# Optimization experiments

Hardware: AMD Instinct MI355X
Metric: run time of the kernel (lower is better)

Reference implementation:

```python
import jax, jax.numpy as jnp
import numpy as np

B, NQ, NV, DIM, HEADS, K = 2, 2048, 2048, 256, 8, 8
HD = DIM // HEADS
HID = 4 * DIM
SCALE = HD ** -0.5
EPS = 1e-5


def setup_inputs() -> dict:
    key = jax.random.key(0)
    ks = jax.random.split(key, 40)
    r = lambda i, s: jax.random.normal(ks[i], s, jnp.float32) * 0.02
    inp = {
        'q': jax.random.normal(ks[0], (B, NQ, DIM), jnp.float32),
        'v': jax.random.normal(ks[1], (B, NV, DIM), jnp.float32),
        'q_pos': jax.random.normal(ks[2], (B, NQ, 3), jnp.float32),
        'v_pos': jax.random.normal(ks[3], (B, NV, 3), jnp.float32),
        'self_knn_index': jax.random.randint(ks[4], (B, NQ, K), 0, NQ, jnp.int32),
        'cross_knn_index': jax.random.randint(ks[5], (B, NQ, K), 0, NV, jnp.int32),
        # LayerNorms (gamma=1, beta=0)
        'norm1_g': jnp.ones(DIM), 'norm1_b': jnp.zeros(DIM),
        'normq_g': jnp.ones(DIM), 'normq_b': jnp.zeros(DIM),
        'normv_g': jnp.ones(DIM), 'normv_b': jnp.zeros(DIM),
        'norm2_g': jnp.ones(DIM), 'norm2_b': jnp.zeros(DIM),
        # self-attention (qkv_bias=False), proj has bias
        'sa_qkv_w': r(6, (DIM, 3 * DIM)),
        'sa_proj_w': r(7, (DIM, DIM)), 'sa_proj_b': jnp.zeros(DIM),
        # cross-attention: q proj and kv proj (no bias), out proj with bias
        'ca_q_w': r(8, (DIM, DIM)),
        'ca_kv_w': r(9, (DIM, 2 * DIM)),
        'ca_proj_w': r(10, (DIM, DIM)), 'ca_proj_b': jnp.zeros(DIM),
        # MLP
        'fc1_w': r(11, (DIM, HID)), 'fc1_b': jnp.zeros(HID),
        'fc2_w': r(12, (HID, DIM)), 'fc2_b': jnp.zeros(DIM),
        # kNN maps
        'knn_w': r(13, (2 * DIM, DIM)), 'knn_b': jnp.zeros(DIM),
        'merge_w': r(14, (2 * DIM, DIM)), 'merge_b': jnp.zeros(DIM),
        'knnx_w': r(15, (2 * DIM, DIM)), 'knnx_b': jnp.zeros(DIM),
        'mergex_w': r(16, (2 * DIM, DIM)), 'mergex_b': jnp.zeros(DIM),
    }
    return inp


def _ln(x, g, b):
    m = x.mean(-1, keepdims=True)
    var = x.var(-1, keepdims=True)
    return (x - m) / jnp.sqrt(var + EPS) * g + b


def _heads(x):  # [B,N,DIM] -> [B,H,N,HD]
    Bx, N, _ = x.shape
    return x.reshape(Bx, N, HEADS, HD).transpose(0, 2, 1, 3)


def _attend(qh, kh, vh, proj_w, proj_b):
    a = jax.nn.softmax(jnp.einsum('bhqd,bhkd->bhqk', qh, kh) * SCALE, axis=-1)
    o = jnp.einsum('bhqk,bhkd->bhqd', a, vh)
    Bx, _, N, _ = o.shape
    o = o.transpose(0, 2, 1, 3).reshape(Bx, N, DIM)
    return o @ proj_w + proj_b


_gather = jax.vmap(lambda pts, idx: pts[idx])  # ([N,D],[Nq,K]) -> [Nq,K,D]


def _knn_feature(qn, vn, idx):  # gather -> diff/cat -> [B,Nq,K,2D]
    local = _gather(vn, idx)                      # [B,Nq,K,D]
    qe = qn[:, :, None, :]                        # [B,Nq,1,D]
    return jnp.concatenate([local - qe, jnp.broadcast_to(qe, local.shape)], -1)


def reference(q, v, q_pos, v_pos, self_knn_index, cross_knn_index,
              norm1_g, norm1_b, normq_g, normq_b, normv_g, normv_b,
              norm2_g, norm2_b, sa_qkv_w, sa_proj_w, sa_proj_b,
              ca_q_w, ca_kv_w, ca_proj_w, ca_proj_b,
              fc1_w, fc1_b, fc2_w, fc2_b,
              knn_w, knn_b, merge_w, merge_b,
              knnx_w, knnx_b, mergex_w, mergex_b):
    # ---- self-attention block with self-kNN branch ----
    nq = _ln(q, norm1_g, norm1_b)
    qkv = nq @ sa_qkv_w
    qh, kh, vh = (_heads(t) for t in jnp.split(qkv, 3, axis=-1))
    sa_out = _attend(qh, kh, vh, sa_proj_w, sa_proj_b)
    f = _knn_feature(nq, nq, self_knn_index)
    knn_out = jax.nn.leaky_relu(f @ knn_w + knn_b, 0.2).max(axis=-2)
    q1 = jnp.concatenate([sa_out, knn_out], -1) @ merge_w + merge_b
    q = q + q1
    # ---- cross-attention block with cross-kNN branch ----
    nq2 = _ln(q, normq_g, normq_b)
    nv = _ln(v, normv_g, normv_b)
    qh = _heads(nq2 @ ca_q_w)
    kh, vh = (_heads(t) for t in jnp.split(nv @ ca_kv_w, 2, axis=-1))
    ca_out = _attend(qh, kh, vh, ca_proj_w, ca_proj_b)
    f = _knn_feature(nq2, nv, cross_knn_index)
    knnx_out = jax.nn.leaky_relu(f @ knnx_w + knnx_b, 0.2).max(axis=-2)
    q2 = jnp.concatenate([ca_out, knnx_out], -1) @ mergex_w + mergex_b
    q = q + q2
    # ---- MLP block ----
    h = _ln(q, norm2_g, norm2_b)
    h = jax.nn.gelu(h @ fc1_w + fc1_b, approximate=False)
    q = q + (h @ fc2_w + fc2_b)
    return q
```

## Files before the change

kernel.cpp:

```cpp
#include <hip/hip_runtime.h>
#include <math.h>

#define NQC   2048
#define NKVC  2048
#define DIMC  256
#define SCALEF 0.17677669529663687f

typedef short bfrag __attribute__((ext_vector_type(8)));
typedef float ffrag __attribute__((ext_vector_type(4)));
typedef unsigned short us8 __attribute__((ext_vector_type(8)));

__device__ __forceinline__ float gelu_exact(float x) {
    return 0.5f * x * (1.0f + erff(x * 0.70710678118654752f));
}
__device__ __forceinline__ unsigned short f2bf(float f) {
    union { float f; unsigned u; } v; v.f = f;
    unsigned r = v.u + 0x7FFFu + ((v.u >> 16) & 1u);
    return (unsigned short)(r >> 16);
}
__device__ __forceinline__ float bf2f(unsigned short u) {
    union { unsigned u; float f; } v; v.u = ((unsigned)u) << 16;
    return v.f;
}

__global__ __launch_bounds__(256) void prep_w(
    const float* __restrict__ qkv, const float* __restrict__ knn,
    const float* __restrict__ proj, const float* __restrict__ merge,
    const float* __restrict__ caq, const float* __restrict__ knnx,
    const float* __restrict__ cakv, const float* __restrict__ projx,
    const float* __restrict__ mergex, const float* __restrict__ fc1,
    const float* __restrict__ fc2, unsigned short* __restrict__ dst)
{
    int e = (blockIdx.x * 256 + threadIdx.x) * 4;
    float v[4];
    float scale = 1.0f;
    if (e < 327680) {
        int n = e >> 8, k = e & 255;
        if (n < 768) {
            const float* s = qkv + (size_t)k * 768 + n;
            #pragma unroll
            for (int i = 0; i < 4; ++i) v[i] = s[(size_t)i * 768];
            if (n < 256) scale = SCALEF;
        } else if (n < 1024) {
            const float* s = knn + (size_t)k * 256 + (n - 768);
            #pragma unroll
            for (int i = 0; i < 4; ++i) v[i] = s[(size_t)i * 256];
        } else {
            const float* s = knn + (size_t)k * 256 + (n - 1024);
            #pragma unroll
            for (int i = 0; i < 4; ++i) v[i] = s[65536 + (size_t)i * 256] - s[(size_t)i * 256];
        }
    } else if (e < 393216) {
        int l = e - 327680, n = l >> 8, k = l & 255;
        const float* s = proj + (size_t)k * 256 + n;
        #pragma unroll
        for (int i = 0; i < 4; ++i) v[i] = s[(size_t)i * 256];
    } else if (e < 524288) {
        int l = e - 393216, n = l >> 9, k = l & 511;
        const float* s = merge + (size_t)k * 256 + n;
        #pragma unroll
        for (int i = 0; i < 4; ++i) v[i] = s[(size_t)i * 256];
    } else if (e < 655360) {
        int l = e - 524288, n = l >> 8, k = l & 255;
        if (n < 256) {
            const float* s = caq + (size_t)k * 256 + n;
            #pragma unroll
            for (int i = 0; i < 4; ++i) v[i] = s[(size_t)i * 256];
            scale = SCALEF;
        } else {
            const float* s = knnx + (size_t)k * 256 + (n - 256);
            #pragma unroll
            for (int i = 0; i < 4; ++i) v[i] = s[65536 + (size_t)i * 256] - s[(size_t)i * 256];
        }
    } else if (e < 851968) {
        int l = e - 655360, n = l >> 8, k = l & 255;
        if (n < 512) {
            const float* s = cakv + (size_t)k * 512 + n;
            #pragma unroll
            for (int i = 0; i < 4; ++i) v[i] = s[(size_t)i * 512];
        } else {
            const float* s = knnx + (size_t)k * 256 + (n - 512);
            #pragma unroll
            for (int i = 0; i < 4; ++i) v[i] = s[(size_t)i * 256];
        }
    } else if (e < 917504) {
        int l = e - 851968, n = l >> 8, k = l & 255;
        const float* s = projx + (size_t)k * 256 + n;
        #pragma unroll
        for (int i = 0; i < 4; ++i) v[i] = s[(size_t)i * 256];
    } else if (e < 1048576) {
        int l = e - 917504, n = l >> 9, k = l & 511;
        const float* s = mergex + (size_t)k * 256 + n;
        #pragma unroll
        for (int i = 0; i < 4; ++i) v[i] = s[(size_t)i * 256];
    } else if (e < 1310720) {
        int l = e - 1048576, n = l >> 8, k = l & 255;
        const float* s = fc1 + (size_t)k * 1024 + n;
        #pragma unroll
        for (int i = 0; i < 4; ++i) v[i] = s[(size_t)i * 1024];
    } else {
        int l = e - 1310720, n = l >> 10, k = l & 1023;
        const float* s = fc2 + (size_t)k * 256 + n;
        #pragma unroll
        for (int i = 0; i < 4; ++i) v[i] = s[(size_t)i * 256];
    }
    ushort4 o;
    o.x = f2bf(v[0] * scale); o.y = f2bf(v[1] * scale);
    o.z = f2bf(v[2] * scale); o.w = f2bf(v[3] * scale);
    *(ushort4*)(dst + e) = o;
}

__global__ __launch_bounds__(256) void ln_b(
    const float* __restrict__ x, const float* __restrict__ g,
    const float* __restrict__ b, unsigned short* __restrict__ y)
{
    int wid = threadIdx.x >> 6, lane = threadIdx.x & 63;
    int row = blockIdx.x * 4 + wid;
    const float* xr = x + (size_t)row * DIMC + lane * 4;
    float4 vv = *(const float4*)xr;
    float s  = vv.x + vv.y + vv.z + vv.w;
    float sq = vv.x*vv.x + vv.y*vv.y + vv.z*vv.z + vv.w*vv.w;
    #pragma unroll
    for (int off = 32; off >= 1; off >>= 1) {
        s  += __shfl_xor(s, off);
        sq += __shfl_xor(sq, off);
    }
    float mean = s * (1.0f/DIMC);
    float var  = sq * (1.0f/DIMC) - mean*mean;
    float inv  = rsqrtf(var + 1e-5f);
    float4 gg = *(const float4*)(g + lane*4);
    float4 bb = *(const float4*)(b + lane*4);
    ushort4 o;
    o.x = f2bf((vv.x - mean) * inv * gg.x + bb.x);
    o.y = f2bf((vv.y - mean) * inv * gg.y + bb.y);
    o.z = f2bf((vv.z - mean) * inv * gg.z + bb.z);
    o.w = f2bf((vv.w - mean) * inv * gg.w + bb.w);
    *(ushort4*)(y + (size_t)row * DIMC + lane * 4) = o;
}

template<int ACT>
__global__ __launch_bounds__(256) void gemm128(
    const unsigned short* __restrict__ A, int lda,
    const unsigned short* __restrict__ Wt,
    const float* __restrict__ bias,
    unsigned short* __restrict__ C, int ldc, int Kc)
{
    __shared__ unsigned short Alds[128][40];
    __shared__ unsigned short Wlds[128][40];
    const int tid = threadIdx.x;
    const int wid = tid >> 6, lane = tid & 63;
    const int lm = lane & 15, quad = lane >> 4;
    const int wr = wid >> 1, wc = wid & 1;
    const int row0 = blockIdx.y * 128, col0 = blockIdx.x * 128;
    const int ar = tid >> 1, ac = (tid & 1) * 16;
    const unsigned short* Ag = A  + (size_t)(row0 + ar) * lda + ac;
    const unsigned short* Wg = Wt + (size_t)(col0 + ar) * Kc  + ac;

    us8 a0 = *(const us8*)Ag;
    us8 a1 = *(const us8*)(Ag + 8);
    us8 w0 = *(const us8*)Wg;
    us8 w1 = *(const us8*)(Wg + 8);

    ffrag acc[4][4];
    #pragma unroll
    for (int mi = 0; mi < 4; ++mi)
        #pragma unroll
        for (int ni = 0; ni < 4; ++ni)
            acc[mi][ni] = (ffrag){0.f, 0.f, 0.f, 0.f};

    for (int k0 = 0;;) {
        __syncthreads();
        *(us8*)&Alds[ar][ac]   = a0;
        *(us8*)&Alds[ar][ac+8] = a1;
        *(us8*)&Wlds[ar][ac]   = w0;
        *(us8*)&Wlds[ar][ac+8] = w1;
        __syncthreads();
        k0 += 32;
        if (k0 < Kc) {
            a0 = *(const us8*)(Ag + k0);
            a1 = *(const us8*)(Ag + k0 + 8);
            w0 = *(const us8*)(Wg + k0);
            w1 = *(const us8*)(Wg + k0 + 8);
        }
        bfrag af[4], bw[4];
        #pragma unroll
        for (int mi = 0; mi < 4; ++mi)
            af[mi] = *(const bfrag*)&Alds[wr*64 + mi*16 + lm][quad*8];
        #pragma unroll
        for (int ni = 0; ni < 4; ++ni)
            bw[ni] = *(const bfrag*)&Wlds[wc*64 + ni*16 + lm][quad*8];
        #pragma unroll
        for (int mi = 0; mi < 4; ++mi)
            #pragma unroll
            for (int ni = 0; ni < 4; ++ni)
                acc[mi][ni] = __builtin_amdgcn_mfma_f32_16x16x32_bf16(
                    af[mi], bw[ni], acc[mi][ni], 0, 0, 0);
        if (k0 >= Kc) break;
    }
    #pragma unroll
    for (int mi = 0; mi < 4; ++mi) {
        #pragma unroll
        for (int ni = 0; ni < 4; ++ni) {
            int gr = row0 + wr*64 + mi*16 + quad*4;
            int gc = col0 + wc*64 + ni*16 + lm;
            float bv = bias ? bias[gc] : 0.f;
            #pragma unroll
            for (int r = 0; r < 4; ++r) {
                float o = acc[mi][ni][r] + bv;
                if (ACT == 1) o = gelu_exact(o);
                C[(size_t)(gr + r) * ldc + gc] = f2bf(o);
            }
        }
    }
}

template<int ACT, int RESID, int OUTBF>
__global__ __launch_bounds__(256) void gemm64(
    const unsigned short* __restrict__ A, int lda,
    const unsigned short* __restrict__ Wt,
    const float* __restrict__ bias,
    const float* __restrict__ resid, int ldr,
    void* __restrict__ Cp, int ldc, int Kc)
{
    __shared__ unsigned short Alds[64][72];
    __shared__ unsigned short Wlds[64][72];
    const int tid = threadIdx.x;
    const int wid = tid >> 6, lane = tid & 63;
    const int lm = lane & 15, quad = lane >> 4;
    const int wr = wid >> 1, wc = wid & 1;
    const int row0 = blockIdx.y * 64, col0 = blockIdx.x * 64;
    const int ar = tid >> 2, ac = (tid & 3) * 16;
    const unsigned short* Ag = A  + (size_t)(row0 + ar) * lda + ac;
    const unsigned short* Wg = Wt + (size_t)(col0 + ar) * Kc  + ac;

    us8 a0 = *(const us8*)Ag;
    us8 a1 = *(const us8*)(Ag + 8);
    us8 w0 = *(const us8*)Wg;
    us8 w1 = *(const us8*)(Wg + 8);

    ffrag acc[2][2];
    #pragma unroll
    for (int mi = 0; mi < 2; ++mi)
        #pragma unroll
        for (int ni = 0; ni < 2; ++ni)
            acc[mi][ni] = (ffrag){0.f, 0.f, 0.f, 0.f};

    for (int k0 = 0;;) {
        __syncthreads();
        *(us8*)&Alds[ar][ac]   = a0;
        *(us8*)&Alds[ar][ac+8] = a1;
        *(us8*)&Wlds[ar][ac]   = w0;
        *(us8*)&Wlds[ar][ac+8] = w1;
        __syncthreads();
        k0 += 64;
        if (k0 < Kc) {
            a0 = *(const us8*)(Ag + k0);
            a1 = *(const us8*)(Ag + k0 + 8);
            w0 = *(const us8*)(Wg + k0);
            w1 = *(const us8*)(Wg + k0 + 8);
        }
        #pragma unroll
        for (int kc = 0; kc < 2; ++kc) {
            bfrag af[2], bw[2];
            #pragma unroll
            for (int mi = 0; mi < 2; ++mi)
                af[mi] = *(const bfrag*)&Alds[wr*32 + mi*16 + lm][kc*32 + quad*8];
            #pragma unroll
            for (int ni = 0; ni < 2; ++ni)
                bw[ni] = *(const bfrag*)&Wlds[wc*32 + ni*16 + lm][kc*32 + quad*8];
            #pragma unroll
            for (int mi = 0; mi < 2; ++mi)
                #pragma unroll
                for (int ni = 0; ni < 2; ++ni)
                    acc[mi][ni] = __builtin_amdgcn_mfma_f32_16x16x32_bf16(
                        af[mi], bw[ni], acc[mi][ni], 0, 0, 0);
        }
        if (k0 >= Kc) break;
    }
    #pragma unroll
    for (int mi = 0; mi < 2; ++mi) {
        #pragma unroll
        for (int ni = 0; ni < 2; ++ni) {
            int gr = row0 + wr*32 + mi*16 + quad*4;
            int gc = col0 + wc*32 + ni*16 + lm;
            float bv = bias ? bias[gc] : 0.f;
            #pragma unroll
            for (int r = 0; r < 4; ++r) {
                float o = acc[mi][ni][r] + bv;
                if (ACT == 1) o = gelu_exact(o);
                if (RESID) o += resid[(size_t)(gr + r) * ldr + gc];
                if (OUTBF) ((unsigned short*)Cp)[(size_t)(gr + r) * ldc + gc] = f2bf(o);
                else       ((float*)Cp)[(size_t)(gr + r) * ldc + gc] = o;
            }
        }
    }
}

__global__ __launch_bounds__(256) void gemm64_comb(
    const unsigned short* __restrict__ Op, const float* __restrict__ Lp,
    const unsigned short* __restrict__ Wt,
    const float* __restrict__ bias,
    unsigned short* __restrict__ C, int ldc)
{
    __shared__ unsigned short Alds[64][72];
    __shared__ unsigned short Wlds[64][72];
    const int tid = threadIdx.x;
    const int wid = tid >> 6, lane = tid & 63;
    const int lm = lane & 15, quad = lane >> 4;
    const int wr = wid >> 1, wc = wid & 1;
    const int row0 = blockIdx.y * 64, col0 = blockIdx.x * 64;
    const int ar = tid >> 2, ac = (tid & 3) * 16;
    const int grow = row0 + ar;
    const unsigned short* O0 = Op + (size_t)grow * 256 + ac;
    const unsigned short* O1 = Op + (size_t)(4096 + grow) * 256 + ac;
    const float* L0 = Lp + (size_t)grow * 8;
    const float* L1 = Lp + (size_t)(4096 + grow) * 8;
    const unsigned short* Wg = Wt + (size_t)(col0 + ar) * 256 + ac;

    us8 o00 = *(const us8*)O0;
    us8 o01 = *(const us8*)(O0 + 8);
    us8 o10 = *(const us8*)O1;
    us8 o11 = *(const us8*)(O1 + 8);
    float li = 1.0f / (L0[ac >> 5] + L1[ac >> 5]);
    us8 w0 = *(const us8*)Wg;
    us8 w1 = *(const us8*)(Wg + 8);

    ffrag acc[2][2];
    #pragma unroll
    for (int mi = 0; mi < 2; ++mi)
        #pragma unroll
        for (int ni = 0; ni < 2; ++ni)
            acc[mi][ni] = (ffrag){0.f, 0.f, 0.f, 0.f};

    for (int k0 = 0;;) {
        us8 ac0, ac1;
        #pragma unroll
        for (int i = 0; i < 8; ++i) {
            ac0[i] = f2bf((bf2f(o00[i]) + bf2f(o10[i])) * li);
            ac1[i] = f2bf((bf2f(o01[i]) + bf2f(o11[i])) * li);
        }
        __syncthreads();
        *(us8*)&Alds[ar][ac]   = ac0;
        *(us8*)&Alds[ar][ac+8] = ac1;
        *(us8*)&Wlds[ar][ac]   = w0;
        *(us8*)&Wlds[ar][ac+8] = w1;
        __syncthreads();
        k0 += 64;
        if (k0 < 256) {
            o00 = *(const us8*)(O0 + k0);
            o01 = *(const us8*)(O0 + k0 + 8);
            o10 = *(const us8*)(O1 + k0);
            o11 = *(const us8*)(O1 + k0 + 8);
            li = 1.0f / (L0[(k0 + ac) >> 5] + L1[(k0 + ac) >> 5]);
            w0 = *(const us8*)(Wg + k0);
            w1 = *(const us8*)(Wg + k0 + 8);
        }
        #pragma unroll
        for (int kc = 0; kc < 2; ++kc) {
            bfrag af[2], bw[2];
            #pragma unroll
            for (int mi = 0; mi < 2; ++mi)
                af[mi] = *(const bfrag*)&Alds[wr*32 + mi*16 + lm][kc*32 + quad*8];
            #pragma unroll
            for (int ni = 0; ni < 2; ++ni)
                bw[ni] = *(const bfrag*)&Wlds[wc*32 + ni*16 + lm][kc*32 + quad*8];
            #pragma unroll
            for (int mi = 0; mi < 2; ++mi)
                #pragma unroll
                for (int ni = 0; ni < 2; ++ni)
                    acc[mi][ni] = __builtin_amdgcn_mfma_f32_16x16x32_bf16(
                        af[mi], bw[ni], acc[mi][ni], 0, 0, 0);
        }
        if (k0 >= 256) break;
    }
    #pragma unroll
    for (int mi = 0; mi < 2; ++mi) {
        #pragma unroll
        for (int ni = 0; ni < 2; ++ni) {
            int gr = row0 + wr*32 + mi*16 + quad*4;
            int gc = col0 + wc*32 + ni*16 + lm;
            float bv = bias[gc];
            #pragma unroll
            for (int r = 0; r < 4; ++r)
                C[(size_t)(gr + r) * ldc + gc] = f2bf(acc[mi][ni][r] + bv);
        }
    }
}

__global__ __launch_bounds__(256) void attn_part(
    const unsigned short* __restrict__ Qp, int ldq,
    const unsigned short* __restrict__ Kp, int ldk,
    const unsigned short* __restrict__ Vp, int ldv,
    unsigned short* __restrict__ Op, float* __restrict__ Lp)
{
    __shared__ unsigned short Klds[64][40];
    __shared__ unsigned short Vt[32][72];
    __shared__ unsigned short Plds[4][16][72];
    int zc = blockIdx.z, bb = zc >> 1, ck = zc & 1;
    int h = blockIdx.y;
    int hoff = h * 32;
    int tid = threadIdx.x, wid = tid >> 6, lane = tid & 63;
    int lm = lane & 15, quad = lane >> 4;
    size_t qbase  = (size_t)bb * NQC;
    size_t kvbase = (size_t)bb * NKVC;
    int q0 = blockIdx.x * 64 + wid * 16;

    bfrag aq = *(const bfrag*)(Qp + (qbase + q0 + lm) * (size_t)ldq + hoff + quad * 8);

    float l_r[4] = {0.f, 0.f, 0.f, 0.f};
    ffrag oacc[2];
    oacc[0] = (ffrag){0.f, 0.f, 0.f, 0.f};
    oacc[1] = (ffrag){0.f, 0.f, 0.f, 0.f};

    const int kkey = tid >> 2, kd0 = (tid & 3) * 8;
    const int vkey = tid & 63, vd0 = (tid >> 6) * 8;
    const unsigned short* kg0 = Kp + (kvbase + kkey) * (size_t)ldk + hoff + kd0;
    const unsigned short* vg0 = Vp + (kvbase + vkey) * (size_t)ldv + hoff + vd0;

    for (int kt = ck * 16; kt < ck * 16 + 16; ++kt) {
        us8 kv = *(const us8*)(kg0 + (size_t)kt * 64 * ldk);
        us8 vv = *(const us8*)(vg0 + (size_t)kt * 64 * ldv);
        __syncthreads();
        *(us8*)&Klds[kkey][kd0] = kv;
        #pragma unroll
        for (int i = 0; i < 8; ++i) Vt[vd0 + i][vkey] = vv[i];
        __syncthreads();

        ffrag sacc[4];
        #pragma unroll
        for (int t = 0; t < 4; ++t) {
            bfrag bk = *(const bfrag*)&Klds[t*16 + lm][quad * 8];
            sacc[t] = __builtin_amdgcn_mfma_f32_16x16x32_bf16(
                aq, bk, (ffrag){0.f,0.f,0.f,0.f}, 0, 0, 0);
        }

        #pragma unroll
        for (int r = 0; r < 4; ++r) {
            float p0 = __expf(sacc[0][r]), p1 = __expf(sacc[1][r]);
            float p2 = __expf(sacc[2][r]), p3 = __expf(sacc[3][r]);
            l_r[r] += (p0 + p1) + (p2 + p3);
            int row = quad * 4 + r;
            Plds[wid][row][lm +  0] = f2bf(p0);
            Plds[wid][row][lm + 16] = f2bf(p1);
            Plds[wid][row][lm + 32] = f2bf(p2);
            Plds[wid][row][lm + 48] = f2bf(p3);
        }
        asm volatile("s_waitcnt lgkmcnt(0)" ::: "memory");

        #pragma unroll
        for (int kc = 0; kc < 2; ++kc) {
            bfrag ap = *(const bfrag*)&Plds[wid][lm][kc*32 + quad*8];
            #pragma unroll
            for (int nt = 0; nt < 2; ++nt) {
                bfrag bv = *(const bfrag*)&Vt[nt*16 + lm][kc*32 + quad*8];
                oacc[nt] = __builtin_amdgcn_mfma_f32_16x16x32_bf16(
                    ap, bv, oacc[nt], 0, 0, 0);
            }
        }
    }
    #pragma unroll
    for (int nt = 0; nt < 2; ++nt)
        #pragma unroll
        for (int r = 0; r < 4; ++r)
            Op[((size_t)ck * 4096 + qbase + q0 + quad*4 + r) * 256 + hoff + nt*16 + lm]
                = f2bf(oacc[nt][r]);
    #pragma unroll
    for (int r = 0; r < 4; ++r) {
        float l = l_r[r];
        l += __shfl_xor(l, 1);
        l += __shfl_xor(l, 2);
        l += __shfl_xor(l, 4);
        l += __shfl_xor(l, 8);
        if (lm == 0)
            Lp[((size_t)ck * 4096 + qbase + q0 + quad*4 + r) * 8 + h] = l;
    }
}

__global__ __launch_bounds__(256) void gathermax_b(
    const unsigned short* __restrict__ P, int ldp,
    const unsigned short* __restrict__ Base, int ldb,
    const float* __restrict__ bias, const int* __restrict__ idx,
    unsigned short* __restrict__ out, int ldo)
{
    int wid = threadIdx.x >> 6, lane = threadIdx.x & 63;
    int q = blockIdx.x * 4 + wid;
    int b = q >> 11;
    int c = lane * 4;
    ushort4 bu = *(const ushort4*)(Base + (size_t)q * ldb + c);
    float4 bi = *(const float4*)(bias + c);
    float bsx = bf2f(bu.x) + bi.x, bsy = bf2f(bu.y) + bi.y;
    float bsz = bf2f(bu.z) + bi.z, bsw = bf2f(bu.w) + bi.w;
    float4 acc = make_float4(-3e38f, -3e38f, -3e38f, -3e38f);
    const int* ip = idx + (size_t)q * 8;
    #pragma unroll
    for (int k = 0; k < 8; ++k) {
        int j = ip[k];
        ushort4 pu = *(const ushort4*)(P + ((size_t)(b * NKVC + j)) * ldp + c);
        float t;
        t = bsx + bf2f(pu.x); t = t > 0.f ? t : 0.2f * t; acc.x = fmaxf(acc.x, t);
        t = bsy + bf2f(pu.y); t = t > 0.f ? t : 0.2f * t; acc.y = fmaxf(acc.y, t);
        t = bsz + bf2f(pu.z); t = t > 0.f ? t : 0.2f * t; acc.z = fmaxf(acc.z, t);
        t = bsw + bf2f(pu.w); t = t > 0.f ? t : 0.2f * t; acc.w = fmaxf(acc.w, t);
    }
    ushort4 o;
    o.x = f2bf(acc.x); o.y = f2bf(acc.y); o.z = f2bf(acc.z); o.w = f2bf(acc.w);
    *(ushort4*)(out + (size_t)q * ldo + c) = o;
}

extern "C" void kernel_launch(void* const* d_in, const int* in_sizes, int n_in,
                              void* d_out, int out_size, void* d_ws, size_t ws_size,
                              hipStream_t stream) {
    const float* q_in   = (const float*)d_in[0];
    const float* v_in   = (const float*)d_in[1];
    const int*   idx_s  = (const int*)d_in[4];
    const int*   idx_x  = (const int*)d_in[5];
    const float* n1g = (const float*)d_in[6],  *n1b = (const float*)d_in[7];
    const float* nqg = (const float*)d_in[8],  *nqb = (const float*)d_in[9];
    const float* nvg = (const float*)d_in[10], *nvb = (const float*)d_in[11];
    const float* n2g = (const float*)d_in[12], *n2b = (const float*)d_in[13];
    const float* sa_qkv_w  = (const float*)d_in[14];
    const float* sa_proj_w = (const float*)d_in[15];
    const float* sa_proj_b = (const float*)d_in[16];
    const float* ca_q_w    = (const float*)d_in[17];
    const float* ca_kv_w   = (const float*)d_in[18];
    const float* ca_proj_w = (const float*)d_in[19];
    const float* ca_proj_b = (const float*)d_in[20];
    const float* fc1_w = (const float*)d_in[21], *fc1_b = (const float*)d_in[22];
    const float* fc2_w = (const float*)d_in[23], *fc2_b = (const float*)d_in[24];
    const float* knn_w   = (const float*)d_in[25], *knn_b   = (const float*)d_in[26];
    const float* merge_w = (const float*)d_in[27], *merge_b = (const float*)d_in[28];
    const float* knnx_w  = (const float*)d_in[29], *knnx_b  = (const float*)d_in[30];
    const float* mergex_w = (const float*)d_in[31], *mergex_b = (const float*)d_in[32];
    float* out = (float*)d_out;

    unsigned short* A1      = (unsigned short*)d_ws;
    unsigned short* A2      = A1;
    unsigned short* A3      = A1 + (size_t)4096 * 512;
    unsigned short* Hb      = A1;
    unsigned short* CC      = A1 + (size_t)4096 * 1280;
    unsigned short* XB      = CC + (size_t)4096 * 512;
    unsigned short* NVB     = XB + (size_t)4096 * 256;
    unsigned short* WT      = NVB + (size_t)4096 * 256;
    unsigned short* WT1     = WT;
    unsigned short* WTproj  = WT + 327680;
    unsigned short* WTmerge = WT + 393216;
    unsigned short* WT2     = WT + 524288;
    unsigned short* WT3     = WT + 655360;
    unsigned short* WTprojx = WT + 851968;
    unsigned short* WTmergex= WT + 917504;
    unsigned short* WTfc1   = WT + 1048576;
    unsigned short* WTfc2   = WT + 1310720;
    unsigned short* Opart   = WT + 1572864;
    float* Lpart = (float*)(Opart + (size_t)2 * 4096 * 256);

    dim3 blk(256);
    dim3 gAttn(NQC / 64, 8, 4);

    prep_w<<<dim3(1536), blk, 0, stream>>>(sa_qkv_w, knn_w, sa_proj_w, merge_w,
        ca_q_w, knnx_w, ca_kv_w, ca_proj_w, mergex_w, fc1_w, fc2_w, WT);

    ln_b<<<dim3(1024), blk, 0, stream>>>(q_in, n1g, n1b, XB);
    gemm128<0><<<dim3(10,32), blk, 0, stream>>>(XB, 256, WT1,
        nullptr, A1, 1280, 256);
    attn_part<<<gAttn, blk, 0, stream>>>(A1, 1280, A1+256, 1280, A1+512, 1280,
        Opart, Lpart);
    gathermax_b<<<dim3(1024), blk, 0, stream>>>(A1+768, 1280, A1+1024, 1280,
        knn_b, idx_s, CC+256, 512);
    gemm64_comb<<<dim3(4,64), blk, 0, stream>>>(Opart, Lpart, WTproj,
        sa_proj_b, CC, 512);
    gemm64<0,1,0><<<dim3(4,64), blk, 0, stream>>>(CC, 512, WTmerge,
        merge_b, q_in, 256, out, 256, 512);

    ln_b<<<dim3(1024), blk, 0, stream>>>(out, nqg, nqb, XB);
    ln_b<<<dim3(1024), blk, 0, stream>>>(v_in, nvg, nvb, NVB);
    gemm64<0,0,1><<<dim3(8,64), blk, 0, stream>>>(XB, 256, WT2,
        nullptr, nullptr, 0, A2, 512, 256);
    gemm128<0><<<dim3(6,32), blk, 0, stream>>>(NVB, 256, WT3,
        nullptr, A3, 768, 256);
    attn_part<<<gAttn, blk, 0, stream>>>(A2, 512, A3, 768, A3+256, 768,
        Opart, Lpart);
    gathermax_b<<<dim3(1024), blk, 0, stream>>>(A3+512, 768, A2+256, 512,
        knnx_b, idx_x, CC+256, 512);
    gemm64_comb<<<dim3(4,64), blk, 0, stream>>>(Opart, Lpart, WTprojx,
        ca_proj_b, CC, 512);
    gemm64<0,1,0><<<dim3(4,64), blk, 0, stream>>>(CC, 512, WTmergex,
        mergex_b, out, 256, out, 256, 512);

    ln_b<<<dim3(1024), blk, 0, stream>>>(out, n2g, n2b, XB);
    gemm128<1><<<dim3(8,32), blk, 0, stream>>>(XB, 256, WTfc1,
        fc1_b, Hb, 1024, 256);
    gemm64<0,1,0><<<dim3(4,64), blk, 0, stream>>>(Hb, 1024, WTfc2,
        fc2_b, out, 256, out, 256, 1024);
}
```

Measured before the change: 286.2 us.

## Merge independent launches into combined kernels and switch GEMMs to 64-tile variant

Several independent kernels are now issued as one launch by splitting the grid between roles. Weight prep runs alongside the first LayerNorm, the two cross-attention LayerNorms share a launch, the q and kv projections share a dual GEMM, and the attention partials run alongside the kNN gather-max. The 128x128 GEMM is replaced by the 64x64 tiled GEMM, giving more blocks on the large projections and fc1. The aim is to cut launch overhead and idle tails between small kernels. The cost is lower per-block data reuse in the GEMMs, plus heterogeneous blocks inside one grid.

```diff
diff --git a/kernel.cpp b/kernel.cpp
--- a/kernel.cpp
+++ b/kernel.cpp
@@ -23,99 +23,11 @@
     return v.f;
 }
 
-__global__ __launch_bounds__(256) void prep_w(
-    const float* __restrict__ qkv, const float* __restrict__ knn,
-    const float* __restrict__ proj, const float* __restrict__ merge,
-    const float* __restrict__ caq, const float* __restrict__ knnx,
-    const float* __restrict__ cakv, const float* __restrict__ projx,
-    const float* __restrict__ mergex, const float* __restrict__ fc1,
-    const float* __restrict__ fc2, unsigned short* __restrict__ dst)
-{
-    int e = (blockIdx.x * 256 + threadIdx.x) * 4;
-    float v[4];
-    float scale = 1.0f;
-    if (e < 327680) {
-        int n = e >> 8, k = e & 255;
-        if (n < 768) {
-            const float* s = qkv + (size_t)k * 768 + n;
-            #pragma unroll
-            for (int i = 0; i < 4; ++i) v[i] = s[(size_t)i * 768];
-            if (n < 256) scale = SCALEF;
-        } else if (n < 1024) {
-            const float* s = knn + (size_t)k * 256 + (n - 768);
-            #pragma unroll
-            for (int i = 0; i < 4; ++i) v[i] = s[(size_t)i * 256];
-        } else {
-            const float* s = knn + (size_t)k * 256 + (n - 1024);
-            #pragma unroll
-            for (int i = 0; i < 4; ++i) v[i] = s[65536 + (size_t)i * 256] - s[(size_t)i * 256];
-        }
-    } else if (e < 393216) {
-        int l = e - 327680, n = l >> 8, k = l & 255;
-        const float* s = proj + (size_t)k * 256 + n;
-        #pragma unroll
-        for (int i = 0; i < 4; ++i) v[i] = s[(size_t)i * 256];
-    } else if (e < 524288) {
-        int l = e - 393216, n = l >> 9, k = l & 511;
-        const float* s = merge + (size_t)k * 256 + n;
-        #pragma unroll
-        for (int i = 0; i < 4; ++i) v[i] = s[(size_t)i * 256];
-    } else if (e < 655360) {
-        int l = e - 524288, n = l >> 8, k = l & 255;
-        if (n < 256) {
-            const float* s = caq + (size_t)k * 256 + n;
-            #pragma unroll
-            for (int i = 0; i < 4; ++i) v[i] = s[(size_t)i * 256];
-            scale = SCALEF;
-        } else {
-            const float* s = knnx + (size_t)k * 256 + (n - 256);
-            #pragma unroll
-            for (int i = 0; i < 4; ++i) v[i] = s[65536 + (size_t)i * 256] - s[(size_t)i * 256];
-        }
-    } else if (e < 851968) {
-        int l = e - 655360, n = l >> 8, k = l & 255;
-        if (n < 512) {
-            const float* s = cakv + (size_t)k * 512 + n;
-            #pragma unroll
-            for (int i = 0; i < 4; ++i) v[i] = s[(size_t)i * 512];
-        } else {
-            const float* s = knnx + (size_t)k * 256 + (n - 512);
-            #pragma unroll
-            for (int i = 0; i < 4; ++i) v[i] = s[(size_t)i * 256];
-        }
-    } else if (e < 917504) {
-        int l = e - 851968, n = l >> 8, k = l & 255;
-        const float* s = projx + (size_t)k * 256 + n;
-        #pragma unroll
-        for (int i = 0; i < 4; ++i) v[i] = s[(size_t)i * 256];
-    } else if (e < 1048576) {
-        int l = e - 917504, n = l >> 9, k = l & 511;
-        const float* s = mergex + (size_t)k * 256 + n;
-        #pragma unroll
-        for (int i = 0; i < 4; ++i) v[i] = s[(size_t)i * 256];
-    } else if (e < 1310720) {
-        int l = e - 1048576, n = l >> 8, k = l & 255;
-        const float* s = fc1 + (size_t)k * 1024 + n;
-        #pragma unroll
-        for (int i = 0; i < 4; ++i) v[i] = s[(size_t)i * 1024];
-    } else {
-        int l = e - 1310720, n = l >> 10, k = l & 1023;
-        const float* s = fc2 + (size_t)k * 256 + n;
-        #pragma unroll
-        for (int i = 0; i < 4; ++i) v[i] = s[(size_t)i * 256];
-    }
-    ushort4 o;
-    o.x = f2bf(v[0] * scale); o.y = f2bf(v[1] * scale);
-    o.z = f2bf(v[2] * scale); o.w = f2bf(v[3] * scale);
-    *(ushort4*)(dst + e) = o;
-}
-
-__global__ __launch_bounds__(256) void ln_b(
+__device__ __forceinline__ void ln_row(
     const float* __restrict__ x, const float* __restrict__ g,
-    const float* __restrict__ b, unsigned short* __restrict__ y)
-{
-    int wid = threadIdx.x >> 6, lane = threadIdx.x & 63;
-    int row = blockIdx.x * 4 + wid;
+    const float* __restrict__ b, unsigned short* __restrict__ y, int row)
+{
+    int lane = threadIdx.x & 63;
     const float* xr = x + (size_t)row * DIMC + lane * 4;
     float4 vv = *(const float4*)xr;
     float s  = vv.x + vv.y + vv.z + vv.w;
@@ -126,8 +38,7 @@
         sq += __shfl_xor(sq, off);
     }
     float mean = s * (1.0f/DIMC);
-    float var  = sq * (1.0f/DIMC) - mean*mean;
-    float inv  = rsqrtf(var + 1e-5f);
+    float inv  = rsqrtf(sq * (1.0f/DIMC) - mean*mean + 1e-5f);
     float4 gg = *(const float4*)(g + lane*4);
     float4 bb = *(const float4*)(b + lane*4);
     ushort4 o;
@@ -138,80 +49,117 @@
     *(ushort4*)(y + (size_t)row * DIMC + lane * 4) = o;
 }
 
-template<int ACT>
-__global__ __launch_bounds__(256) void gemm128(
-    const unsigned short* __restrict__ A, int lda,
-    const unsigned short* __restrict__ Wt,
-    const float* __restrict__ bias,
-    unsigned short* __restrict__ C, int ldc, int Kc)
-{
-    __shared__ unsigned short Alds[128][40];
-    __shared__ unsigned short Wlds[128][40];
-    const int tid = threadIdx.x;
-    const int wid = tid >> 6, lane = tid & 63;
-    const int lm = lane & 15, quad = lane >> 4;
-    const int wr = wid >> 1, wc = wid & 1;
-    const int row0 = blockIdx.y * 128, col0 = blockIdx.x * 128;
-    const int ar = tid >> 1, ac = (tid & 1) * 16;
-    const unsigned short* Ag = A  + (size_t)(row0 + ar) * lda + ac;
-    const unsigned short* Wg = Wt + (size_t)(col0 + ar) * Kc  + ac;
-
-    us8 a0 = *(const us8*)Ag;
-    us8 a1 = *(const us8*)(Ag + 8);
-    us8 w0 = *(const us8*)Wg;
-    us8 w1 = *(const us8*)(Wg + 8);
-
-    ffrag acc[4][4];
-    #pragma unroll
-    for (int mi = 0; mi < 4; ++mi)
-        #pragma unroll
-        for (int ni = 0; ni < 4; ++ni)
-            acc[mi][ni] = (ffrag){0.f, 0.f, 0.f, 0.f};
-
-    for (int k0 = 0;;) {
-        __syncthreads();
-        *(us8*)&Alds[ar][ac]   = a0;
-        *(us8*)&Alds[ar][ac+8] = a1;
-        *(us8*)&Wlds[ar][ac]   = w0;
-        *(us8*)&Wlds[ar][ac+8] = w1;
-        __syncthreads();
-        k0 += 32;
-        if (k0 < Kc) {
-            a0 = *(const us8*)(Ag + k0);
-            a1 = *(const us8*)(Ag + k0 + 8);
-            w0 = *(const us8*)(Wg + k0);
-            w1 = *(const us8*)(Wg + k0 + 8);
-        }
-        bfrag af[4], bw[4];
-        #pragma unroll
-        for (int mi = 0; mi < 4; ++mi)
-            af[mi] = *(const bfrag*)&Alds[wr*64 + mi*16 + lm][quad*8];
-        #pragma unroll
-        for (int ni = 0; ni < 4; ++ni)
-            bw[ni] = *(const bfrag*)&Wlds[wc*64 + ni*16 + lm][quad*8];
-        #pragma unroll
-        for (int mi = 0; mi < 4; ++mi)
-            #pragma unroll
-            for (int ni = 0; ni < 4; ++ni)
-                acc[mi][ni] = __builtin_amdgcn_mfma_f32_16x16x32_bf16(
-                    af[mi], bw[ni], acc[mi][ni], 0, 0, 0);
-        if (k0 >= Kc) break;
-    }
-    #pragma unroll
-    for (int mi = 0; mi < 4; ++mi) {
-        #pragma unroll
-        for (int ni = 0; ni < 4; ++ni) {
-            int gr = row0 + wr*64 + mi*16 + quad*4;
-            int gc = col0 + wc*64 + ni*16 + lm;
-            float bv = bias ? bias[gc] : 0.f;
-            #pragma unroll
-            for (int r = 0; r < 4; ++r) {
-                float o = acc[mi][ni][r] + bv;
-                if (ACT == 1) o = gelu_exact(o);
-                C[(size_t)(gr + r) * ldc + gc] = f2bf(o);
-            }
-        }
-    }
+__global__ __launch_bounds__(256) void prep_ln(
+    const float* __restrict__ qkv, const float* __restrict__ knn,
+    const float* __restrict__ proj, const float* __restrict__ merge,
+    const float* __restrict__ caq, const float* __restrict__ knnx,
+    const float* __restrict__ cakv, const float* __restrict__ projx,
+    const float* __restrict__ mergex, const float* __restrict__ fc1,
+    const float* __restrict__ fc2, unsigned short* __restrict__ dst,
+    const float* __restrict__ lx, const float* __restrict__ lg,
+    const float* __restrict__ lb, unsigned short* __restrict__ ly)
+{
+    if (blockIdx.x >= 1536) {
+        int row = (blockIdx.x - 1536) * 4 + (threadIdx.x >> 6);
+        ln_row(lx, lg, lb, ly, row);
+        return;
+    }
+    int e = (blockIdx.x * 256 + threadIdx.x) * 4;
+    float v[4];
+    float scale = 1.0f;
+    if (e < 327680) {
+        int n = e >> 8, k = e & 255;
+        if (n < 768) {
+            const float* s = qkv + (size_t)k * 768 + n;
+            #pragma unroll
+            for (int i = 0; i < 4; ++i) v[i] = s[(size_t)i * 768];
+            if (n < 256) scale = SCALEF;
+        } else if (n < 1024) {
+            const float* s = knn + (size_t)k * 256 + (n - 768);
+            #pragma unroll
+            for (int i = 0; i < 4; ++i) v[i] = s[(size_t)i * 256];
+        } else {
+            const float* s = knn + (size_t)k * 256 + (n - 1024);
+            #pragma unroll
+            for (int i = 0; i < 4; ++i) v[i] = s[65536 + (size_t)i * 256] - s[(size_t)i * 256];
+        }
+    } else if (e < 393216) {
+        int l = e - 327680, n = l >> 8, k = l & 255;
+        const float* s = proj + (size_t)k * 256 + n;
+        #pragma unroll
+        for (int i = 0; i < 4; ++i) v[i] = s[(size_t)i * 256];
+    } else if (e < 524288) {
+        int l = e - 393216, n = l >> 9, k = l & 511;
+        const float* s = merge + (size_t)k * 256 + n;
+        #pragma unroll
+        for (int i = 0; i < 4; ++i) v[i] = s[(size_t)i * 256];
+    } else if (e < 655360) {
+        int l = e - 524288, n = l >> 8, k = l & 255;
+        if (n < 256) {
+            const float* s = caq + (size_t)k * 256 + n;
+            #pragma unroll
+            for (int i = 0; i < 4; ++i) v[i] = s[(size_t)i * 256];
+            scale = SCALEF;
+        } else {
+            const float* s = knnx + (size_t)k * 256 + (n - 256);
+            #pragma unroll
+            for (int i = 0; i < 4; ++i) v[i] = s[65536 + (size_t)i * 256] - s[(size_t)i * 256];
+        }
+    } else if (e < 851968) {
+        int l = e - 655360, n = l >> 8, k = l & 255;
+        if (n < 512) {
+            const float* s = cakv + (size_t)k * 512 + n;
+            #pragma unroll
+            for (int i = 0; i < 4; ++i) v[i] = s[(size_t)i * 512];
+        } else {
+            const float* s = knnx + (size_t)k * 256 + (n - 512);
+            #pragma unroll
+            for (int i = 0; i < 4; ++i) v[i] = s[(size_t)i * 256];
+        }
+    } else if (e < 917504) {
+        int l = e - 851968, n = l >> 8, k = l & 255;
+        const float* s = projx + (size_t)k * 256 + n;
+        #pragma unroll
+        for (int i = 0; i < 4; ++i) v[i] = s[(size_t)i * 256];
+    } else if (e < 1048576) {
+        int l = e - 917504, n = l >> 9, k = l & 511;
+        const float* s = mergex + (size_t)k * 256 + n;
+        #pragma unroll
+        for (int i = 0; i < 4; ++i) v[i] = s[(size_t)i * 256];
+    } else if (e < 1310720) {
+        int l = e - 1048576, n = l >> 8, k = l & 255;
+        const float* s = fc1 + (size_t)k * 1024 + n;
+        #pragma unroll
+        for (int i = 0; i < 4; ++i) v[i] = s[(size_t)i * 1024];
+    } else {
+        int l = e - 1310720, n = l >> 10, k = l & 1023;
+        const float* s = fc2 + (size_t)k * 256 + n;
+        #pragma unroll
+        for (int i = 0; i < 4; ++i) v[i] = s[(size_t)i * 256];
+    }
+    ushort4 o;
+    o.x = f2bf(v[0] * scale); o.y = f2bf(v[1] * scale);
+    o.z = f2bf(v[2] * scale); o.w = f2bf(v[3] * scale);
+    *(ushort4*)(dst + e) = o;
+}
+
+__global__ __launch_bounds__(256) void ln2_b(
+    const float* __restrict__ x1, const float* __restrict__ g1,
+    const float* __restrict__ b1, unsigned short* __restrict__ y1,
+    const float* __restrict__ x2, const float* __restrict__ g2,
+    const float* __restrict__ b2, unsigned short* __restrict__ y2)
+{
+    int wid = threadIdx.x >> 6;
+    int blk = blockIdx.x;
+    if (blk < 1024) ln_row(x1, g1, b1, y1, blk * 4 + wid);
+    else            ln_row(x2, g2, b2, y2, (blk - 1024) * 4 + wid);
+}
+
+__global__ __launch_bounds__(256) void ln_b(
+    const float* __restrict__ x, const float* __restrict__ g,
+    const float* __restrict__ b, unsigned short* __restrict__ y)
+{
+    ln_row(x, g, b, y, blockIdx.x * 4 + (threadIdx.x >> 6));
 }
 
 template<int ACT, int RESID, int OUTBF>
@@ -292,6 +240,87 @@
                 if (OUTBF) ((unsigned short*)Cp)[(size_t)(gr + r) * ldc + gc] = f2bf(o);
                 else       ((float*)Cp)[(size_t)(gr + r) * ldc + gc] = o;
             }
+        }
+    }
+}
+
+__global__ __launch_bounds__(256) void gemm64_dual(
+    const unsigned short* __restrict__ XB,
+    const unsigned short* __restrict__ NVB,
+    const unsigned short* __restrict__ WT2,
+    const unsigned short* __restrict__ WT3,
+    unsigned short* __restrict__ A2,
+    unsigned short* __restrict__ A3)
+{
+    const unsigned short* A; const unsigned short* Wt;
+    unsigned short* C; int ldc, col0;
+    if (blockIdx.x < 8) { A = XB;  Wt = WT2; C = A2; ldc = 512; col0 = blockIdx.x * 64; }
+    else                { A = NVB; Wt = WT3; C = A3; ldc = 768; col0 = (blockIdx.x - 8) * 64; }
+
+    __shared__ unsigned short Alds[64][72];
+    __shared__ unsigned short Wlds[64][72];
+    const int tid = threadIdx.x;
+    const int wid = tid >> 6, lane = tid & 63;
+    const int lm = lane & 15, quad = lane >> 4;
+    const int wr = wid >> 1, wc = wid & 1;
+    const int row0 = blockIdx.y * 64;
+    const int ar = tid >> 2, ac = (tid & 3) * 16;
+    const unsigned short* Ag = A  + (size_t)(row0 + ar) * 256 + ac;
+    const unsigned short* Wg = Wt + (size_t)(col0 + ar) * 256 + ac;
+
+    us8 a0 = *(const us8*)Ag;
+    us8 a1 = *(const us8*)(Ag + 8);
+    us8 w0 = *(const us8*)Wg;
+    us8 w1 = *(const us8*)(Wg + 8);
+
+    ffrag acc[2][2];
+    #pragma unroll
+    for (int mi = 0; mi < 2; ++mi)
+        #pragma unroll
+        for (int ni = 0; ni < 2; ++ni)
+            acc[mi][ni] = (ffrag){0.f, 0.f, 0.f, 0.f};
+
+    for (int k0 = 0;;) {
+        __syncthreads();
+        *(us8*)&Alds[ar][ac]   = a0;
+        *(us8*)&Alds[ar][ac+8] = a1;
+        *(us8*)&Wlds[ar][ac]   = w0;
+        *(us8*)&Wlds[ar][ac+8] = w1;
+        __syncthreads();
+        k0 += 64;
+        if (k0 < 256) {
+            a0 = *(const us8*)(Ag + k0);
+            a1 = *(const us8*)(Ag + k0 + 8);
+            w0 = *(const us8*)(Wg + k0);
+            w1 = *(const us8*)(Wg + k0 + 8);
+        }
+        #pragma unroll
+        for (int kc = 0; kc < 2; ++kc) {
+            bfrag af[2], bw[2];
+            #pragma unroll
+            for (int mi = 0; mi < 2; ++mi)
+                af[mi] = *(const bfrag*)&Alds[wr*32 + mi*16 + lm][kc*32 + quad*8];
+            #pragma unroll
+            for (int ni = 0; ni < 2; ++ni)
+                bw[ni] = *(const bfrag*)&Wlds[wc*32 + ni*16 + lm][kc*32 + quad*8];
+            #pragma unroll
+            for (int mi = 0; mi < 2; ++mi)
+                #pragma unroll
+                for (int ni = 0; ni < 2; ++ni)
+                    acc[mi][ni] = __builtin_amdgcn_mfma_f32_16x16x32_bf16(
+                        af[mi], bw[ni], acc[mi][ni], 0, 0, 0);
+        }
+        if (k0 >= 256) break;
+    }
+    #pragma unroll
+    for (int mi = 0; mi < 2; ++mi) {
+        #pragma unroll
+        for (int ni = 0; ni < 2; ++ni) {
+            int gr = row0 + wr*32 + mi*16 + quad*4;
+            int gc = col0 + wc*32 + ni*16 + lm;
+            #pragma unroll
+            for (int r = 0; r < 4; ++r)
+                C[(size_t)(gr + r) * ldc + gc] = f2bf(acc[mi][ni][r]);
         }
     }
 }
@@ -387,19 +416,51 @@
     }
 }
 
-__global__ __launch_bounds__(256) void attn_part(
+__global__ __launch_bounds__(256) void attn_gather(
     const unsigned short* __restrict__ Qp, int ldq,
     const unsigned short* __restrict__ Kp, int ldk,
     const unsigned short* __restrict__ Vp, int ldv,
-    unsigned short* __restrict__ Op, float* __restrict__ Lp)
+    unsigned short* __restrict__ Op, float* __restrict__ Lp,
+    const unsigned short* __restrict__ P, int ldp,
+    const unsigned short* __restrict__ Base, int ldb,
+    const float* __restrict__ gbias, const int* __restrict__ idx,
+    unsigned short* __restrict__ gout, int ldgo)
 {
     __shared__ unsigned short Klds[64][40];
     __shared__ unsigned short Vt[32][72];
     __shared__ unsigned short Plds[4][16][72];
+    int tid = threadIdx.x, wid = tid >> 6, lane = tid & 63;
+
+    if (blockIdx.z >= 4) {
+        int gbid = blockIdx.x + 32 * (blockIdx.y + 8 * (blockIdx.z - 4));
+        int q = gbid * 4 + wid;
+        int b = q >> 11;
+        int c = lane * 4;
+        ushort4 bu = *(const ushort4*)(Base + (size_t)q * ldb + c);
+        float4 bi = *(const float4*)(gbias + c);
+        float bsx = bf2f(bu.x) + bi.x, bsy = bf2f(bu.y) + bi.y;
+        float bsz = bf2f(bu.z) + bi.z, bsw = bf2f(bu.w) + bi.w;
+        float4 acc = make_float4(-3e38f, -3e38f, -3e38f, -3e38f);
+        const int* ip = idx + (size_t)q * 8;
+        #pragma unroll
+        for (int k = 0; k < 8; ++k) {
+            int j = ip[k];
+            ushort4 pu = *(const ushort4*)(P + ((size_t)(b * NKVC + j)) * ldp + c);
+            float t;
+            t = bsx + bf2f(pu.x); t = t > 0.f ? t : 0.2f * t; acc.x = fmaxf(acc.x, t);
+            t = bsy + bf2f(pu.y); t = t > 0.f ? t : 0.2f * t; acc.y = fmaxf(acc.y, t);
+            t = bsz + bf2f(pu.z); t = t > 0.f ? t : 0.2f * t; acc.z = fmaxf(acc.z, t);
+            t = bsw + bf2f(pu.w); t = t > 0.f ? t : 0.2f * t; acc.w = fmaxf(acc.w, t);
+        }
+        ushort4 o;
+        o.x = f2bf(acc.x); o.y = f2bf(acc.y); o.z = f2bf(acc.z); o.w = f2bf(acc.w);
+        *(ushort4*)(gout + (size_t)q * ldgo + c) = o;
+        return;
+    }
+
     int zc = blockIdx.z, bb = zc >> 1, ck = zc & 1;
     int h = blockIdx.y;
     int hoff = h * 32;
-    int tid = threadIdx.x, wid = tid >> 6, lane = tid & 63;
     int lm = lane & 15, quad = lane >> 4;
     size_t qbase  = (size_t)bb * NQC;
     size_t kvbase = (size_t)bb * NKVC;
@@ -474,37 +535,6 @@
         if (lm == 0)
             Lp[((size_t)ck * 4096 + qbase + q0 + quad*4 + r) * 8 + h] = l;
     }
-}
-
-__global__ __launch_bounds__(256) void gathermax_b(
-    const unsigned short* __restrict__ P, int ldp,
-    const unsigned short* __restrict__ Base, int ldb,
-    const float* __restrict__ bias, const int* __restrict__ idx,
-    unsigned short* __restrict__ out, int ldo)
-{
-    int wid = threadIdx.x >> 6, lane = threadIdx.x & 63;
-    int q = blockIdx.x * 4 + wid;
-    int b = q >> 11;
-    int c = lane * 4;
-    ushort4 bu = *(const ushort4*)(Base + (size_t)q * ldb + c);
-    float4 bi = *(const float4*)(bias + c);
-    float bsx = bf2f(bu.x) + bi.x, bsy = bf2f(bu.y) + bi.y;
-    float bsz = bf2f(bu.z) + bi.z, bsw = bf2f(bu.w) + bi.w;
-    float4 acc = make_float4(-3e38f, -3e38f, -3e38f, -3e38f);
-    const int* ip = idx + (size_t)q * 8;
-    #pragma unroll
-    for (int k = 0; k < 8; ++k) {
-        int j = ip[k];
-        ushort4 pu = *(const ushort4*)(P + ((size_t)(b * NKVC + j)) * ldp + c);
-        float t;
-        t = bsx + bf2f(pu.x); t = t > 0.f ? t : 0.2f * t; acc.x = fmaxf(acc.x, t);
-        t = bsy + bf2f(pu.y); t = t > 0.f ? t : 0.2f * t; acc.y = fmaxf(acc.y, t);
-        t = bsz + bf2f(pu.z); t = t > 0.f ? t : 0.2f * t; acc.z = fmaxf(acc.z, t);
-        t = bsw + bf2f(pu.w); t = t > 0.f ? t : 0.2f * t; acc.w = fmaxf(acc.w, t);
-    }
-    ushort4 o;
-    o.x = f2bf(acc.x); o.y = f2bf(acc.y); o.z = f2bf(acc.z); o.w = f2bf(acc.w);
-    *(ushort4*)(out + (size_t)q * ldo + c) = o;
 }
 
 extern "C" void kernel_launch(void* const* d_in, const int* in_sizes, int n_in,
@@ -554,41 +584,34 @@
     float* Lpart = (float*)(Opart + (size_t)2 * 4096 * 256);
 
     dim3 blk(256);
-    dim3 gAttn(NQC / 64, 8, 4);
-
-    prep_w<<<dim3(1536), blk, 0, stream>>>(sa_qkv_w, knn_w, sa_proj_w, merge_w,
-        ca_q_w, knnx_w, ca_kv_w, ca_proj_w, mergex_w, fc1_w, fc2_w, WT);
-
-    ln_b<<<dim3(1024), blk, 0, stream>>>(q_in, n1g, n1b, XB);
-    gemm128<0><<<dim3(10,32), blk, 0, stream>>>(XB, 256, WT1,
-        nullptr, A1, 1280, 256);
-    attn_part<<<gAttn, blk, 0, stream>>>(A1, 1280, A1+256, 1280, A1+512, 1280,
-        Opart, Lpart);
-    gathermax_b<<<dim3(1024), blk, 0, stream>>>(A1+768, 1280, A1+1024, 1280,
-        knn_b, idx_s, CC+256, 512);
+    dim3 gAG(NQC / 64, 8, 8);
+
+    prep_ln<<<dim3(2560), blk, 0, stream>>>(sa_qkv_w, knn_w, sa_proj_w, merge_w,
+        ca_q_w, knnx_w, ca_kv_w, ca_proj_w, mergex_w, fc1_w, fc2_w, WT,
+        q_in, n1g, n1b, XB);
+
+    gemm64<0,0,1><<<dim3(20,64), blk, 0, stream>>>(XB, 256, WT1,
+        nullptr, nullptr, 0, A1, 1280, 256);
+    attn_gather<<<gAG, blk, 0, stream>>>(A1, 1280, A1+256, 1280, A1+512, 1280,
+        Opart, Lpart, A1+768, 1280, A1+1024, 1280, knn_b, idx_s, CC+256, 512);
     gemm64_comb<<<dim3(4,64), blk, 0, stream>>>(Opart, Lpart, WTproj,
         sa_proj_b, CC, 512);
     gemm64<0,1,0><<<dim3(4,64), blk, 0, stream>>>(CC, 512, WTmerge,
         merge_b, q_in, 256, out, 256, 512);
 
-    ln_b<<<dim3(1024), blk, 0, stream>>>(out, nqg, nqb, XB);
-    ln_b<<<dim3(1024), blk, 0, stream>>>(v_in, nvg, nvb, NVB);
-    gemm64<0,0,1><<<dim3(8,64), blk, 0, stream>>>(XB, 256, WT2,
-        nullptr, nullptr, 0, A2, 512, 256);
-    gemm128<0><<<dim3(6,32), blk, 0, stream>>>(NVB, 256, WT3,
-        nullptr, A3, 768, 256);
-    attn_part<<<gAttn, blk, 0, stream>>>(A2, 512, A3, 768, A3+256, 768,
-        Opart, Lpart);
-    gathermax_b<<<dim3(1024), blk, 0, stream>>>(A3+512, 768, A2+256, 512,
-        knnx_b, idx_x, CC+256, 512);
+    ln2_b<<<dim3(2048), blk, 0, stream>>>(out, nqg, nqb, XB,
+        v_in, nvg, nvb, NVB);
+    gemm64_dual<<<dim3(20,64), blk, 0, stream>>>(XB, NVB, WT2, WT3, A2, A3);
+    attn_gather<<<gAG, blk, 0, stream>>>(A2, 512, A3, 768, A3+256, 768,
+        Opart, Lpart, A3+512, 768, A2+256, 512, knnx_b, idx_x, CC+256, 512);
     gemm64_comb<<<dim3(4,64), blk, 0, stream>>>(Opart, Lpart, WTprojx,
         ca_proj_b, CC, 512);
     gemm64<0,1,0><<<dim3(4,64), blk, 0, stream>>>(CC, 512, WTmergex,
         mergex_b, out, 256, out, 256, 512);
 
     ln_b<<<dim3(1024), blk, 0, stream>>>(out, n2g, n2b, XB);
-    gemm128<1><<<dim3(8,32), blk, 0, stream>>>(XB, 256, WTfc1,
-        fc1_b, Hb, 1024, 256);
+    gemm64<1,0,1><<<dim3(16,64), blk, 0, stream>>>(XB, 256, WTfc1,
+        fc1_b, nullptr, 0, Hb, 1024, 256);
     gemm64<0,1,0><<<dim3(4,64), blk, 0, stream>>>(Hb, 1024, WTfc2,
         fc2_b, out, 256, out, 256, 1024);
 }
```

Measured after the change: 261.4 us. -8.7%, faster.
